# Performance work log

Measured on AMD Instinct MI355X. Metric: run time of the kernel, lower is better.

Reference implementation:

```python
import jax, jax.numpy as jnp
import numpy as np

B, S, H, NH, HD = 2, 2048, 4096, 32, 128  # batch, seq, hidden, heads, head_dim
THETA = 10000.0
SCALE = HD ** -0.5


def setup_inputs() -> dict:
    key = jax.random.key(0)
    k1, k2, k3 = jax.random.split(key, 3)
    hidden_states = jax.random.normal(k1, (B, S, H), jnp.float32) * 0.02
    w_pack = jax.random.normal(k2, (3 * H, H), jnp.float32) * 0.02  # fused QKV weight
    w_o = jax.random.normal(k3, (H, H), jnp.float32) * 0.02
    positions = jnp.broadcast_to(jnp.arange(S, dtype=jnp.int32), (B, S))
    return {"positions": positions, "hidden_states": hidden_states,
            "w_pack": w_pack, "w_o": w_o}


def _apply_rope(x, positions):
    # x: [B, S, NH, HD]; neox-style (rotate-half) RoPE over full head_dim
    inv_freq = 1.0 / (THETA ** (jnp.arange(0, HD, 2, dtype=jnp.float32) / HD))  # [HD/2]
    ang = positions.astype(jnp.float32)[..., None] * inv_freq  # [B, S, HD/2]
    cos = jnp.cos(ang)[:, :, None, :]  # [B, S, 1, HD/2]
    sin = jnp.sin(ang)[:, :, None, :]
    x1, x2 = x[..., : HD // 2], x[..., HD // 2 :]
    return jnp.concatenate([x1 * cos - x2 * sin, x2 * cos + x1 * sin], axis=-1)


def reference(positions, hidden_states, w_pack, w_o):
    # Fused QKV projection then split (W_pack, bias-free)
    qkv = jnp.einsum('bsh,oh->bso', hidden_states, w_pack)  # [B, S, 3H]
    q, k, v = jnp.split(qkv, 3, axis=-1)
    q = q.reshape(B, S, NH, HD)
    k = k.reshape(B, S, NH, HD)
    v = v.reshape(B, S, NH, HD)
    q = _apply_rope(q, positions)
    k = _apply_rope(k, positions)
    # Causal scaled-dot-product attention
    scores = jnp.einsum('bqhd,bkhd->bhqk', q, k) * SCALE
    causal = jnp.tril(jnp.ones((S, S), dtype=bool))
    scores = jnp.where(causal, scores, jnp.float32(-1e9))
    probs = jax.nn.softmax(scores, axis=-1)
    attn = jnp.einsum('bhqk,bkhd->bqhd', probs, v).reshape(B, S, H)
    return jnp.einsum('bsh,oh->bso', attn, w_o)  # o_proj, bias-free
```

## Files before the change

kernel.cpp:

```cpp
#include <hip/hip_runtime.h>

typedef short short8 __attribute__((ext_vector_type(8)));
typedef float f32x4 __attribute__((ext_vector_type(4)));
typedef unsigned short u16;

static constexpr int BATCH = 2, S = 2048, H = 4096, NHEAD = 32, HDIM = 128;

__device__ __forceinline__ u16 f2b(float f) {
  union { float f; unsigned u; } v; v.f = f;
  return (u16)((v.u + 0x7fffu + ((v.u >> 16) & 1u)) >> 16);
}
__device__ __forceinline__ float b2f(u16 h) {
  union { unsigned u; float f; } v; v.u = ((unsigned)h) << 16;
  return v.f;
}

__device__ __forceinline__ void gl16(const u16* g, u16* l) {
  __builtin_amdgcn_global_load_lds((__attribute__((address_space(1))) void*)g,
                                   (__attribute__((address_space(3))) void*)l,
                                   16, 0, 0);
}

#define MFMA(acc, a, b) \
  acc = __builtin_amdgcn_mfma_f32_16x16x32_bf16(a, b, acc, 0, 0, 0)

__global__ __launch_bounds__(256) void cvt_bf16(const float* __restrict__ in,
                                                u16* __restrict__ out) {
  size_t i = ((size_t)blockIdx.x * 256 + threadIdx.x) * 4;
  float4 v = *(const float4*)(in + i);
  ushort4 o = { f2b(v.x), f2b(v.y), f2b(v.z), f2b(v.w) };
  *(ushort4*)(out + i) = o;
}

__global__ __launch_bounds__(256) void rope_table(float* __restrict__ tab) {
  int idx = blockIdx.x * 256 + threadIdx.x;
  int p = idx >> 6, f = idx & 63;
  float freq = __powf(10000.0f, -(float)f * (1.0f / 64.0f));
  float a = (float)p * freq;
  tab[(size_t)p * 128 + f] = cosf(a);
  tab[(size_t)p * 128 + 64 + f] = sinf(a);
}

template <int MODE>
__global__ __launch_bounds__(512, 2) void gemm256(
    const u16* __restrict__ A, const u16* __restrict__ B, void* __restrict__ C,
    int M, int N, int K, const int* __restrict__ pos,
    const float* __restrict__ tab, u16* __restrict__ qr, u16* __restrict__ kr,
    u16* __restrict__ vt) {
  __shared__ u16 SMEM[69632];
  u16* AL = SMEM;
  u16* BL = SMEM + 32768;
  const int nbn = N >> 8;
  const int nwg = (M >> 8) * nbn;
  const int bid = blockIdx.x;
  const int wg = (bid & 7) * (nwg >> 3) + (bid >> 3);
  const int bm = wg / nbn, bn = wg % nbn;
  const int tid = threadIdx.x, lane = tid & 63;
  const int w = tid >> 6, wm = w >> 2, wn = w & 3;
  const int hi = lane >> 4, lo = lane & 15;
  const int nk = K >> 6;

  const u16* Abase = A + (size_t)(bm * 256) * K;
  const u16* Bbase = B + (size_t)(bn * 256) * K;

#define STG_A(buf, half, kt)                                                   \
  { _Pragma("unroll") for (int i = 0; i < 2; ++i) {                            \
      int c = tid + i * 512, r = c >> 3, s = c & 7;                            \
      gl16(Abase + (size_t)((half) * 128 + r) * K + (kt) * 64 +                \
               ((s ^ (r & 7)) * 8),                                            \
           &AL[((buf) * 2 + (half)) * 8192 + c * 8]);                          \
    } }
#define STG_B(buf, half, kt)                                                   \
  { _Pragma("unroll") for (int i = 0; i < 2; ++i) {                            \
      int c = tid + i * 512, r = c >> 3, s = c & 7;                            \
      gl16(Bbase + (size_t)((half) * 128 + r) * K + (kt) * 64 +                \
               ((s ^ (r & 7)) * 8),                                            \
           &BL[((buf) * 2 + (half)) * 8192 + c * 8]);                          \
    } }
#define PREBAR()                                                               \
  do { __builtin_amdgcn_sched_barrier(0);                                      \
       __builtin_amdgcn_s_barrier(); } while (0)

  f32x4 acc[8][4] = {};

  STG_A(0, 0, 0) STG_A(0, 1, 0) STG_B(0, 0, 0) STG_B(0, 1, 0)
  if (nk > 1) {
    STG_B(1, 0, 1) STG_B(1, 1, 1)
    asm volatile("s_waitcnt vmcnt(4)" ::: "memory");
  } else {
    asm volatile("s_waitcnt vmcnt(0)" ::: "memory");
  }
  __builtin_amdgcn_sched_barrier(0);
  __builtin_amdgcn_s_barrier();

  short8 af[4][2], bf[2][2][2];

  for (int t = 0; t < nk; ++t) {
    const int cur = t & 1;
    const u16* Awave = AL + (cur * 2 + wm) * 8192;
    const u16* Bwave = BL + (cur * 2 + (wn >> 1)) * 8192;
    const int lrB = (wn & 1) * 64;

#pragma unroll
    for (int mi = 0; mi < 4; ++mi)
#pragma unroll
      for (int ks = 0; ks < 2; ++ks)
        af[mi][ks] = *(const short8*)&Awave[(mi * 16 + lo) * 64 +
                                            (((ks * 4 + hi) ^ (lo & 7)) * 8)];
#pragma unroll
    for (int ni = 0; ni < 2; ++ni)
#pragma unroll
      for (int ks = 0; ks < 2; ++ks)
        bf[0][ni][ks] = *(const short8*)&Bwave[(lrB + ni * 16 + lo) * 64 +
                                               (((ks * 4 + hi) ^ (lo & 7)) * 8)];
    if (t + 1 < nk) STG_A(cur ^ 1, 0, t + 1)
    PREBAR();
    __builtin_amdgcn_s_setprio(1);
#pragma unroll
    for (int mi = 0; mi < 4; ++mi)
#pragma unroll
      for (int ni = 0; ni < 2; ++ni)
#pragma unroll
        for (int ks = 0; ks < 2; ++ks)
          MFMA(acc[mi][ni], af[mi][ks], bf[0][ni][ks]);
    __builtin_amdgcn_s_setprio(0);
    __builtin_amdgcn_s_barrier();

#pragma unroll
    for (int ni = 0; ni < 2; ++ni)
#pragma unroll
      for (int ks = 0; ks < 2; ++ks)
        bf[1][ni][ks] = *(const short8*)&Bwave[(lrB + 32 + ni * 16 + lo) * 64 +
                                               (((ks * 4 + hi) ^ (lo & 7)) * 8)];
    if (t + 1 < nk) STG_A(cur ^ 1, 1, t + 1)
    PREBAR();
    __builtin_amdgcn_s_setprio(1);
#pragma unroll
    for (int mi = 0; mi < 4; ++mi)
#pragma unroll
      for (int ni = 0; ni < 2; ++ni)
#pragma unroll
        for (int ks = 0; ks < 2; ++ks)
          MFMA(acc[mi][2 + ni], af[mi][ks], bf[1][ni][ks]);
    __builtin_amdgcn_s_setprio(0);
    __builtin_amdgcn_s_barrier();

#pragma unroll
    for (int mi = 0; mi < 4; ++mi)
#pragma unroll
      for (int ks = 0; ks < 2; ++ks)
        af[mi][ks] = *(const short8*)&Awave[((64 + mi * 16 + lo)) * 64 +
                                            (((ks * 4 + hi) ^ (lo & 7)) * 8)];
    if (t + 2 < nk) STG_B(cur, 0, t + 2)
    PREBAR();
    __builtin_amdgcn_s_setprio(1);
#pragma unroll
    for (int mi = 0; mi < 4; ++mi)
#pragma unroll
      for (int ni = 0; ni < 2; ++ni)
#pragma unroll
        for (int ks = 0; ks < 2; ++ks)
          MFMA(acc[4 + mi][2 + ni], af[mi][ks], bf[1][ni][ks]);
    __builtin_amdgcn_s_setprio(0);
    __builtin_amdgcn_s_barrier();

    if (t + 2 < nk) {
      STG_B(cur, 1, t + 2)
      asm volatile("s_waitcnt vmcnt(4)" ::: "memory");
    } else {
      asm volatile("s_waitcnt vmcnt(0)" ::: "memory");
    }
    PREBAR();
    __builtin_amdgcn_s_setprio(1);
#pragma unroll
    for (int mi = 0; mi < 4; ++mi)
#pragma unroll
      for (int ni = 0; ni < 2; ++ni)
#pragma unroll
        for (int ks = 0; ks < 2; ++ks)
          MFMA(acc[4 + mi][ni], af[mi][ks], bf[0][ni][ks]);
    __builtin_amdgcn_s_setprio(0);
    __builtin_amdgcn_s_barrier();
  }

  if constexpr (MODE == 1) {
#pragma unroll
    for (int mf = 0; mf < 8; ++mf)
#pragma unroll
      for (int nf = 0; nf < 4; ++nf)
#pragma unroll
        for (int j = 0; j < 4; ++j) {
          size_t idx = (size_t)(bm * 256 + wm * 128 + mf * 16 + hi * 4 + j) * N +
                       bn * 256 + wn * 64 + nf * 16 + lo;
          ((float*)C)[idx] = acc[mf][nf][j];
        }
  } else {
    const int SP = 272;
    u16* E = SMEM;
#pragma unroll
    for (int mf = 0; mf < 8; ++mf)
#pragma unroll
      for (int nf = 0; nf < 4; ++nf)
#pragma unroll
        for (int j = 0; j < 4; ++j)
          E[(wm * 128 + mf * 16 + hi * 4 + j) * SP + wn * 64 + nf * 16 + lo] =
              f2b(acc[mf][nf][j]);
    __syncthreads();

    const int grow0 = bm * 256, gcol0 = bn * 256;
    const int bb = grow0 >> 11, s0 = grow0 & 2047;
    if (gcol0 < 8192) {
      for (int task = tid; task < 8192; task += 512) {
        int row = task >> 5, g = task & 31;
        int gcol = gcol0 + g * 8;
        int d = gcol & 127, f0 = d & 63;
        int p = pos[grow0 + row];
        const float* cp = tab + (size_t)p * 128 + f0;
        float4 ca = *(const float4*)cp, cb = *(const float4*)(cp + 4);
        float4 sa = *(const float4*)(cp + 64), sb = *(const float4*)(cp + 68);
        float cv[8] = {ca.x, ca.y, ca.z, ca.w, cb.x, cb.y, cb.z, cb.w};
        float sv[8] = {sa.x, sa.y, sa.z, sa.w, sb.x, sb.y, sb.z, sb.w};
        short8 x = *(const short8*)&E[row * SP + g * 8];
        short8 xo = *(const short8*)&E[row * SP + (g ^ 8) * 8];
        float sgn = (d < 64) ? -1.0f : 1.0f;
        unsigned word[4];
#pragma unroll
        for (int pr = 0; pr < 4; ++pr) {
          float v0 = b2f((u16)x[2 * pr]) * cv[2 * pr] +
                     sgn * b2f((u16)xo[2 * pr]) * sv[2 * pr];
          float v1 = b2f((u16)x[2 * pr + 1]) * cv[2 * pr + 1] +
                     sgn * b2f((u16)xo[2 * pr + 1]) * sv[2 * pr + 1];
          word[pr] = (unsigned)f2b(v0) | ((unsigned)f2b(v1) << 16);
        }
        int hidx = gcol >> 7;
        u16* outp = (hidx < 32) ? qr : kr;
        int nh = (hidx < 32) ? hidx : hidx - 32;
        size_t dst = ((size_t)(bb * 32 + nh) * 2048 + (s0 + row)) * 128 + d;
        uint4 o = {word[0], word[1], word[2], word[3]};
        *(uint4*)&outp[dst] = o;
      }
    } else {
      for (int task = tid; task < 8192; task += 512) {
        int kbl = task >> 11;
        int hh = (task >> 10) & 1;
        int c = task & 1023;
        int f = c >> 6, l = c & 63;
        int ks2 = f >> 3, db = f & 7, hi2 = l >> 4, lo2 = l & 15;
        int base = (kbl * 64 + ks2 * 32 + hi2 * 8) * SP + hh * 128 + db * 16 + lo2;
        unsigned e0 = E[base], e1 = E[base + SP], e2 = E[base + 2 * SP],
                 e3 = E[base + 3 * SP], e4 = E[base + 4 * SP],
                 e5 = E[base + 5 * SP], e6 = E[base + 6 * SP],
                 e7 = E[base + 7 * SP];
        int nh = ((gcol0 - 8192) >> 7) + hh;
        size_t dst = ((size_t)(bb * 32 + nh) * 2048 + (s0 + kbl * 64)) * 128 +
                     (size_t)c * 8;
        uint4 o = {e0 | (e1 << 16), e2 | (e3 << 16), e4 | (e5 << 16),
                   e6 | (e7 << 16)};
        *(uint4*)&vt[dst] = o;
      }
    }
  }
}

__global__ __launch_bounds__(256, 2) void flash_fwd(const u16* __restrict__ q,
                                                    const u16* __restrict__ k,
                                                    const u16* __restrict__ vt,
                                                    u16* __restrict__ o) {
  __shared__ u16 KB[2][64 * 128];
  __shared__ u16 VB[2][64 * 128];
  __shared__ u16 Ps[4][16 * 64];
  const int nqt = S / 64;
  const int qt = (nqt - 1) - ((int)blockIdx.x % nqt);
  const int bh = blockIdx.x / nqt;
  const int tid = threadIdx.x, lane = tid & 63, w = tid >> 6;
  const int hi = lane >> 4, lo = lane & 15;

  const u16* qg = q + ((size_t)bh * S + qt * 64 + w * 16) * HDIM;
  short8 qf[4];
#pragma unroll
  for (int ks = 0; ks < 4; ++ks) {
    short8 r = *(const short8*)(qg + (size_t)lo * HDIM + ks * 32 + hi * 8);
    union { short8 s; u16 u[8]; } t; t.s = r;
#pragma unroll
    for (int e = 0; e < 8; ++e)
      t.u[e] = f2b(b2f(t.u[e]) * 0.08838834764831845f);
    qf[ks] = t.s;
  }

  float m_i[4], l_i[4];
  f32x4 oacc[8] = {};
#pragma unroll
  for (int j = 0; j < 4; ++j) { m_i[j] = -1e30f; l_i[j] = 0.0f; }

  const u16* kg = k + (size_t)bh * S * HDIM;
  const u16* vg = vt + (size_t)bh * S * HDIM;

#define STAGE(buf, kvbase)                                                  \
  {                                                                         \
    _Pragma("unroll") for (int i = 0; i < 4; ++i) {                         \
      int idx = i * 256 + tid, r = idx >> 4, gd = idx & 15;                 \
      gl16(kg + (size_t)((kvbase) + r) * HDIM + ((gd ^ (r & 7)) * 8),       \
           &KB[buf][idx * 8]);                                              \
    }                                                                       \
    _Pragma("unroll") for (int i = 0; i < 4; ++i) {                         \
      int idx = i * 256 + tid;                                              \
      gl16(vg + (size_t)(kvbase) * HDIM + idx * 8, &VB[buf][idx * 8]);      \
    }                                                                       \
  }

  STAGE(0, 0)
  int cur = 0;
  u16* PsW = &Ps[w][0];

  for (int kvt = 0; kvt <= qt; ++kvt) {
    if (kvt < qt) {
      STAGE(cur ^ 1, (kvt + 1) * 64)
      asm volatile("s_waitcnt vmcnt(8)" ::: "memory");
    } else {
      asm volatile("s_waitcnt vmcnt(0)" ::: "memory");
    }
    __builtin_amdgcn_s_barrier();
    __builtin_amdgcn_sched_barrier(0);
    const u16* Kc = &KB[cur][0];
    const u16* Vc = &VB[cur][0];

    f32x4 sc[4] = {};
#pragma unroll
    for (int ks = 0; ks < 4; ++ks) {
      const int colu = ks * 32 + hi * 8;
#pragma unroll
      for (int cb = 0; cb < 4; ++cb) {
        const int row = cb * 16 + lo;
        short8 kf = *(const short8*)&Kc[row * 128 + (colu ^ ((row & 7) << 3))];
        MFMA(sc[cb], qf[ks], kf);
      }
    }

    const int qrow = qt * 64 + w * 16 + hi * 4;
    const bool diag = (kvt == qt);
#pragma unroll
    for (int cb = 0; cb < 4; ++cb) {
      const int kvc = kvt * 64 + cb * 16 + lo;
#pragma unroll
      for (int j = 0; j < 4; ++j) {
        float sv = sc[cb][j];
        if (diag && kvc > qrow + j) sv = -1e30f;
        sc[cb][j] = sv;
      }
    }
    float rmax[4], rs[4];
#pragma unroll
    for (int j = 0; j < 4; ++j) {
      rmax[j] = fmaxf(fmaxf(sc[0][j], sc[1][j]), fmaxf(sc[2][j], sc[3][j]));
      for (int d = 8; d; d >>= 1) rmax[j] = fmaxf(rmax[j], __shfl_xor(rmax[j], d));
      float mn = fmaxf(m_i[j], rmax[j]);
      float sf = __expf(m_i[j] - mn);
      m_i[j] = mn; l_i[j] *= sf;
#pragma unroll
      for (int db = 0; db < 8; ++db) oacc[db][j] *= sf;
      rs[j] = 0.0f;
    }
#pragma unroll
    for (int cb = 0; cb < 4; ++cb)
#pragma unroll
      for (int j = 0; j < 4; ++j) {
        float p = __expf(sc[cb][j] - m_i[j]);
        sc[cb][j] = p; rs[j] += p;
      }
#pragma unroll
    for (int j = 0; j < 4; ++j) {
      for (int d = 8; d; d >>= 1) rs[j] += __shfl_xor(rs[j], d);
      l_i[j] += rs[j];
    }

#pragma unroll
    for (int cb = 0; cb < 4; ++cb)
#pragma unroll
      for (int j = 0; j < 4; ++j) {
        const int p = hi * 4 + j;
        PsW[p * 64 + ((cb * 16 + lo) ^ ((p & 7) << 3))] = f2b(sc[cb][j]);
      }
    short8 pf0 = *(const short8*)&PsW[lo * 64 + ((hi * 8) ^ ((lo & 7) << 3))];
    short8 pf1 = *(const short8*)&PsW[lo * 64 + ((32 + hi * 8) ^ ((lo & 7) << 3))];

#pragma unroll
    for (int ks2 = 0; ks2 < 2; ++ks2) {
      const short8 pf = ks2 ? pf1 : pf0;
#pragma unroll
      for (int db = 0; db < 8; ++db) {
        short8 vf = *(const short8*)&Vc[((ks2 * 8 + db) * 64 + lane) * 8];
        MFMA(oacc[db], pf, vf);
      }
    }
    __builtin_amdgcn_s_barrier();
    cur ^= 1;
  }

#pragma unroll
  for (int j = 0; j < 4; ++j) {
    float inv = 1.0f / l_i[j];
    int srow = qt * 64 + w * 16 + hi * 4 + j;
    const int b = bh >> 5, nh = bh & 31;
    size_t base = ((size_t)b * S + srow) * H + (size_t)nh * HDIM + lo;
#pragma unroll
    for (int db = 0; db < 8; ++db)
      o[base + db * 16] = f2b(oacc[db][j] * inv);
  }
}

extern "C" void kernel_launch(void* const* d_in, const int* in_sizes, int n_in,
                              void* d_out, int out_size, void* d_ws, size_t ws_size,
                              hipStream_t stream) {
  const int* pos = (const int*)d_in[0];
  const float* hs = (const float*)d_in[1];
  const float* wpack = (const float*)d_in[2];
  const float* wo = (const float*)d_in[3];
  float* out = (float*)d_out;
  char* ws = (char*)d_ws;
  u16* hs_b    = (u16*)(ws + 0UL);
  u16* wpack_b = (u16*)(ws + 33554432UL);
  u16* wo_b    = (u16*)(ws + 134217728UL);
  u16* v_t     = (u16*)(ws + 167772160UL);
  float* tab   = (float*)(ws + 201326592UL);
  u16* q_r     = (u16*)(ws + 268435456UL);
  u16* k_r     = (u16*)(ws + 301989888UL);
  u16* attn_b  = (u16*)(ws + 335544320UL);

  cvt_bf16<<<16384, 256, 0, stream>>>(hs, hs_b);
  cvt_bf16<<<49152, 256, 0, stream>>>(wpack, wpack_b);
  cvt_bf16<<<16384, 256, 0, stream>>>(wo, wo_b);
  rope_table<<<512, 256, 0, stream>>>(tab);
  gemm256<0><<<768, 512, 0, stream>>>(hs_b, wpack_b, nullptr, 4096, 12288, 4096,
                                      pos, tab, q_r, k_r, v_t);
  flash_fwd<<<64 * 32, 256, 0, stream>>>(q_r, k_r, v_t, attn_b);
  gemm256<1><<<256, 512, 0, stream>>>(attn_b, wo_b, out, 4096, 4096, 4096,
                                      nullptr, nullptr, nullptr, nullptr, nullptr);
}
```

Before: 859.0 us.

## Halve barriers per k-step in GEMM main loop with restructured phase schedule

Reworks the four-phase GEMM main loop so each phase begins with a single barrier instead of a pre-barrier plus trailing barrier. Both B fragment halves are loaded up front, and the last two MFMA groups are merged. LDS prefetch stores are moved right after the barriers, and a syncthreads is added before the epilogue reuses shared memory. This aims to cut barrier stalls at the cost of more live registers and less interleaving of LDS reads with MFMAs.

```diff
diff --git a/kernel.cpp b/kernel.cpp
--- a/kernel.cpp
+++ b/kernel.cpp
@@ -77,9 +77,9 @@
                ((s ^ (r & 7)) * 8),                                            \
            &BL[((buf) * 2 + (half)) * 8192 + c * 8]);                          \
     } }
-#define PREBAR()                                                               \
-  do { __builtin_amdgcn_sched_barrier(0);                                      \
-       __builtin_amdgcn_s_barrier(); } while (0)
+#define BARTOP()                                                               \
+  do { __builtin_amdgcn_s_barrier();                                           \
+       __builtin_amdgcn_sched_barrier(0); } while (0)
 
   f32x4 acc[8][4] = {};
 
@@ -91,9 +91,8 @@
     asm volatile("s_waitcnt vmcnt(0)" ::: "memory");
   }
   __builtin_amdgcn_sched_barrier(0);
-  __builtin_amdgcn_s_barrier();
-
-  short8 af[4][2], bf[2][2][2];
+
+  short8 af[4][2], bfA[2][2], bfB[2][2];
 
   for (int t = 0; t < nk; ++t) {
     const int cur = t & 1;
@@ -101,6 +100,8 @@
     const u16* Bwave = BL + (cur * 2 + (wn >> 1)) * 8192;
     const int lrB = (wn & 1) * 64;
 
+    BARTOP();
+    if (t + 1 < nk) STG_A(cur ^ 1, 0, t + 1)
 #pragma unroll
     for (int mi = 0; mi < 4; ++mi)
 #pragma unroll
@@ -111,10 +112,17 @@
     for (int ni = 0; ni < 2; ++ni)
 #pragma unroll
       for (int ks = 0; ks < 2; ++ks)
-        bf[0][ni][ks] = *(const short8*)&Bwave[(lrB + ni * 16 + lo) * 64 +
-                                               (((ks * 4 + hi) ^ (lo & 7)) * 8)];
-    if (t + 1 < nk) STG_A(cur ^ 1, 0, t + 1)
-    PREBAR();
+        bfA[ni][ks] = *(const short8*)&Bwave[(lrB + ni * 16 + lo) * 64 +
+                                             (((ks * 4 + hi) ^ (lo & 7)) * 8)];
+
+    BARTOP();
+    if (t + 1 < nk) STG_A(cur ^ 1, 1, t + 1)
+#pragma unroll
+    for (int ni = 0; ni < 2; ++ni)
+#pragma unroll
+      for (int ks = 0; ks < 2; ++ks)
+        bfB[ni][ks] = *(const short8*)&Bwave[(lrB + 32 + ni * 16 + lo) * 64 +
+                                             (((ks * 4 + hi) ^ (lo & 7)) * 8)];
     __builtin_amdgcn_s_setprio(1);
 #pragma unroll
     for (int mi = 0; mi < 4; ++mi)
@@ -122,18 +130,11 @@
       for (int ni = 0; ni < 2; ++ni)
 #pragma unroll
         for (int ks = 0; ks < 2; ++ks)
-          MFMA(acc[mi][ni], af[mi][ks], bf[0][ni][ks]);
+          MFMA(acc[mi][ni], af[mi][ks], bfA[ni][ks]);
     __builtin_amdgcn_s_setprio(0);
-    __builtin_amdgcn_s_barrier();
-
-#pragma unroll
-    for (int ni = 0; ni < 2; ++ni)
-#pragma unroll
-      for (int ks = 0; ks < 2; ++ks)
-        bf[1][ni][ks] = *(const short8*)&Bwave[(lrB + 32 + ni * 16 + lo) * 64 +
-                                               (((ks * 4 + hi) ^ (lo & 7)) * 8)];
-    if (t + 1 < nk) STG_A(cur ^ 1, 1, t + 1)
-    PREBAR();
+
+    BARTOP();
+    if (t + 2 < nk) STG_B(cur, 0, t + 2)
     __builtin_amdgcn_s_setprio(1);
 #pragma unroll
     for (int mi = 0; mi < 4; ++mi)
@@ -141,18 +142,17 @@
       for (int ni = 0; ni < 2; ++ni)
 #pragma unroll
         for (int ks = 0; ks < 2; ++ks)
-          MFMA(acc[mi][2 + ni], af[mi][ks], bf[1][ni][ks]);
+          MFMA(acc[mi][2 + ni], af[mi][ks], bfB[ni][ks]);
     __builtin_amdgcn_s_setprio(0);
-    __builtin_amdgcn_s_barrier();
-
 #pragma unroll
     for (int mi = 0; mi < 4; ++mi)
 #pragma unroll
       for (int ks = 0; ks < 2; ++ks)
         af[mi][ks] = *(const short8*)&Awave[((64 + mi * 16 + lo)) * 64 +
                                             (((ks * 4 + hi) ^ (lo & 7)) * 8)];
-    if (t + 2 < nk) STG_B(cur, 0, t + 2)
-    PREBAR();
+
+    BARTOP();
+    if (t + 2 < nk) STG_B(cur, 1, t + 2)
     __builtin_amdgcn_s_setprio(1);
 #pragma unroll
     for (int mi = 0; mi < 4; ++mi)
@@ -160,27 +160,21 @@
       for (int ni = 0; ni < 2; ++ni)
 #pragma unroll
         for (int ks = 0; ks < 2; ++ks)
-          MFMA(acc[4 + mi][2 + ni], af[mi][ks], bf[1][ni][ks]);
+          MFMA(acc[4 + mi][2 + ni], af[mi][ks], bfB[ni][ks]);
+#pragma unroll
+    for (int mi = 0; mi < 4; ++mi)
+#pragma unroll
+      for (int ni = 0; ni < 2; ++ni)
+#pragma unroll
+        for (int ks = 0; ks < 2; ++ks)
+          MFMA(acc[4 + mi][ni], af[mi][ks], bfA[ni][ks]);
     __builtin_amdgcn_s_setprio(0);
-    __builtin_amdgcn_s_barrier();
-
     if (t + 2 < nk) {
-      STG_B(cur, 1, t + 2)
       asm volatile("s_waitcnt vmcnt(4)" ::: "memory");
     } else {
       asm volatile("s_waitcnt vmcnt(0)" ::: "memory");
     }
-    PREBAR();
-    __builtin_amdgcn_s_setprio(1);
-#pragma unroll
-    for (int mi = 0; mi < 4; ++mi)
-#pragma unroll
-      for (int ni = 0; ni < 2; ++ni)
-#pragma unroll
-        for (int ks = 0; ks < 2; ++ks)
-          MFMA(acc[4 + mi][ni], af[mi][ks], bf[0][ni][ks]);
-    __builtin_amdgcn_s_setprio(0);
-    __builtin_amdgcn_s_barrier();
+    __builtin_amdgcn_sched_barrier(0);
   }
 
   if constexpr (MODE == 1) {
@@ -197,6 +191,7 @@
   } else {
     const int SP = 272;
     u16* E = SMEM;
+    __syncthreads();
 #pragma unroll
     for (int mf = 0; mf < 8; ++mf)
 #pragma unroll
```

Measured after the change: 855.9 us. No clear change (-0.4%).
